# Kernel tuning notes

Hardware: AMD Instinct MI355X
Metric: run time of the kernel (lower is better)

## Reference

```python
import jax, jax.numpy as jnp
import numpy as np

N = 500_000      # active input voxels
C = 64           # feature channels
B = 2            # batch size
RES = 256        # input spatial resolution (coords in [0, RES))
FACTOR = 2       # downsample factor (init kwarg)


def setup_inputs() -> dict:
    key = jax.random.key(0)
    k1, k2, k3 = jax.random.split(key, 3)
    feats = jax.random.normal(k1, (N, C), dtype=jnp.float32)
    bidx = jax.random.randint(k2, (N, 1), 0, B, dtype=jnp.int32)
    xyz = jax.random.randint(k3, (N, 3), 0, RES, dtype=jnp.int32)
    coords = jnp.concatenate([bidx, xyz], axis=1)  # [N, 4] = (b, x, y, z)
    return {"feats": feats, "coords": coords}


def reference(feats, coords):
    """Sparse voxel downsample: coord hashing + dedup + scatter-mean pooling.

    Returns (new_feats [N, C], new_coords [N, 4]); rows beyond the number of
    unique downsampled voxels are zero-feature / coord = -1 padding (JAX needs
    static shapes; torch original returns only the n_unique valid rows).
    """
    res = RES // FACTOR  # static spatial extent after downsampling
    b = coords[:, 0].astype(jnp.int32)
    xyz = coords[:, 1:] // FACTOR  # [N, 3]
    # linear hash code = ((b*res + x)*res + y)*res + z
    code = ((b * res + xyz[:, 0]) * res + xyz[:, 1]) * res + xyz[:, 2]
    uniq, inv = jnp.unique(code, size=N, fill_value=-1, return_inverse=True)
    # mean pooling with include_self=False == segment_sum / segment_count
    counts = jax.ops.segment_sum(jnp.ones((N,), feats.dtype), inv, num_segments=N)
    sums = jax.ops.segment_sum(feats, inv, num_segments=N)  # [N, C]
    new_feats = sums / jnp.maximum(counts, 1.0)[:, None]
    # decode unique codes back to (b, x, y, z)
    valid = counts > 0
    z = uniq % res
    y = (uniq // res) % res
    x = (uniq // (res * res)) % res
    nb = uniq // (res * res * res)
    new_coords = jnp.stack([nb, x, y, z], axis=-1).astype(jnp.int32)
    new_coords = jnp.where(valid[:, None], new_coords, -1)
    return new_feats, new_coords
```

## Files before the change

### kernel.cpp

```cpp
#include <hip/hip_runtime.h>


#define RES2 128
#define NCODES (2 * 128 * 128 * 128)
#define NW (NCODES / 4)
#define HBLK 4096

typedef float f4 __attribute__((ext_vector_type(4)));

__global__ void zero_cnt(uint4* __restrict__ p) {
    int i = blockIdx.x * 256 + threadIdx.x;
    const uint4 zz = make_uint4(0u, 0u, 0u, 0u);
    if (i < NW / 4) p[i] = zz;
}

__global__ void count_codes(const int* __restrict__ coords,
                            unsigned* __restrict__ cnt8,
                            int* __restrict__ codes, int n) {
    int i = blockIdx.x * 256 + threadIdx.x;
    if (i >= n) return;
    const int4 v = reinterpret_cast<const int4*>(coords)[i];
    int code = (((v.x * RES2 + (v.y >> 1)) * RES2 + (v.z >> 1)) * RES2) + (v.w >> 1);
    codes[i] = code;
    atomicAdd(&cnt8[code >> 2], 1u << (8 * (code & 3)));
}

__global__ void block_flag_sum(const unsigned* __restrict__ cnt8,
                               unsigned* __restrict__ btot) {
    __shared__ unsigned sh[256];
    int t = threadIdx.x;
    unsigned w = cnt8[blockIdx.x * 256 + t];
    sh[t] = ((w & 0xFFu) != 0) + (((w >> 8) & 0xFFu) != 0) +
            (((w >> 16) & 0xFFu) != 0) + ((w >> 24) != 0);
    __syncthreads();
    for (int off = 128; off > 0; off >>= 1) {
        if (t < off) sh[t] += sh[t + off];
        __syncthreads();
    }
    if (t == 0) btot[blockIdx.x] = sh[0];
}

__global__ void scan_totals(unsigned* __restrict__ btot,
                            unsigned* __restrict__ nuq) {
    __shared__ unsigned sh[1024];
    int t = threadIdx.x;
    int base = t * 4;
    unsigned v[4], e[4], s = 0;
#pragma unroll
    for (int j = 0; j < 4; ++j) { v[j] = btot[base + j]; e[j] = s; s += v[j]; }
    sh[t] = s;
    __syncthreads();
    for (int off = 1; off < 1024; off <<= 1) {
        unsigned add = (t >= off) ? sh[t - off] : 0u;
        __syncthreads();
        sh[t] += add;
        __syncthreads();
    }
    unsigned excl = (t == 0) ? 0u : sh[t - 1];
#pragma unroll
    for (int j = 0; j < 4; ++j) btot[base + j] = excl + e[j];
    if (t == 1023) *nuq = sh[1023];
}

__global__ void scan_write(const unsigned* __restrict__ cnt8,
                           const unsigned* __restrict__ btot,
                           unsigned* __restrict__ wprefix,
                           f4* __restrict__ outF4,
                           f4* __restrict__ outC4) {
    __shared__ unsigned sh[256];
    int t = threadIdx.x;
    int widx = blockIdx.x * 256 + t;
    unsigned w = cnt8[widx];
    unsigned c4[4] = {w & 0xFFu, (w >> 8) & 0xFFu, (w >> 16) & 0xFFu, w >> 24};
    unsigned e[4], s = 0;
#pragma unroll
    for (int j = 0; j < 4; ++j) { e[j] = s; s += (c4[j] != 0); }
    sh[t] = s;
    __syncthreads();
    for (int off = 1; off < 256; off <<= 1) {
        unsigned add = (t >= off) ? sh[t - off] : 0u;
        __syncthreads();
        sh[t] += add;
        __syncthreads();
    }
    unsigned texcl = ((t == 0) ? 0u : sh[t - 1]) + btot[blockIdx.x];
    wprefix[widx] = texcl;
    int cbase = widx * 4;
#pragma unroll
    for (int j = 0; j < 4; ++j) {
        if (c4[j]) {
            unsigned r = texcl + e[j];
            int code = cbase + j;
            f4 cv = {(float)(code >> 21), (float)((code >> 14) & 127),
                     (float)((code >> 7) & 127), (float)(code & 127)};
            outC4[r] = cv;
            if (c4[j] >= 2) {
                f4* row = outF4 + (size_t)r * 16;
                const f4 zz = {0.f, 0.f, 0.f, 0.f};
#pragma unroll
                for (int q = 0; q < 16; ++q) row[q] = zz;
            }
        }
    }
}

__global__ void tail_pad(const unsigned* __restrict__ nuq,
                         f4* __restrict__ outF4,
                         f4* __restrict__ outC4, int n) {
    int r = blockIdx.x * 256 + threadIdx.x;
    if (r >= n || r < (int)*nuq) return;
    f4* row = outF4 + (size_t)r * 16;
    const f4 zz = {0.f, 0.f, 0.f, 0.f};
#pragma unroll
    for (int q = 0; q < 16; ++q) row[q] = zz;
    f4 mm = {-1.f, -1.f, -1.f, -1.f};
    outC4[r] = mm;
}

__global__ void scatter8(const f4* __restrict__ feats4,
                         const int* __restrict__ codes,
                         const unsigned* __restrict__ cnt8,
                         const unsigned* __restrict__ wprefix,
                         f4* __restrict__ outF4, int n) {
    int tid = blockIdx.x * 256 + threadIdx.x;
    int lane = threadIdx.x & 63;
    int wave = tid >> 6;
    int q = lane >> 4;
    int sub = lane & 15;
    int ib = wave * 8;

#pragma unroll
    for (int h = 0; h < 2; ++h) {
        int i = ib + h * 4 + q;
        if (i >= n) continue;
        int c = codes[i];
        unsigned w = cnt8[c >> 2];
        unsigned base = wprefix[c >> 2];
        int j = c & 3;
        unsigned cnt = (w >> (8 * j)) & 0xFFu;
        unsigned occ = 0;
        if (j > 0) occ += ((w & 0xFFu) != 0);
        if (j > 1) occ += (((w >> 8) & 0xFFu) != 0);
        if (j > 2) occ += (((w >> 16) & 0xFFu) != 0);
        unsigned r = base + occ;
        f4 v = feats4[(size_t)i * 16 + sub];
        f4* dst = outF4 + (size_t)r * 16 + sub;
        if (cnt == 1) {
            __builtin_nontemporal_store(v, dst);
        } else {
            float sc = 1.0f / (float)cnt;
            float* d = (float*)dst;
            atomicAdd(d + 0, v.x * sc);
            atomicAdd(d + 1, v.y * sc);
            atomicAdd(d + 2, v.z * sc);
            atomicAdd(d + 3, v.w * sc);
        }
    }
}

extern "C" void kernel_launch(void* const* d_in, const int* in_sizes, int n_in,
                              void* d_out, int out_size, void* d_ws, size_t ws_size,
                              hipStream_t stream) {
    const float* feats = (const float*)d_in[0];
    const int* coords = (const int*)d_in[1];
    const int n = in_sizes[1] / 4;

    float* outF = (float*)d_out;
    f4* outF4 = (f4*)outF;
    f4* outC4 = (f4*)(outF + (size_t)n * 64);

    unsigned* cnt8 = (unsigned*)d_ws;
    unsigned* btot = cnt8 + NW;
    unsigned* nuq = btot + HBLK;
    int* codes = (int*)(nuq + 1);
    unsigned* wprefix = (unsigned*)(codes + n);

    zero_cnt<<<2048, 256, 0, stream>>>((uint4*)cnt8);

    count_codes<<<(n + 255) / 256, 256, 0, stream>>>(coords, cnt8, codes, n);
    block_flag_sum<<<HBLK, 256, 0, stream>>>(cnt8, btot);
    scan_totals<<<1, 1024, 0, stream>>>(btot, nuq);
    scan_write<<<HBLK, 256, 0, stream>>>(cnt8, btot, wprefix, outF4, outC4);
    tail_pad<<<(n + 255) / 256, 256, 0, stream>>>(nuq, outF4, outC4, n);

    int waves = (n + 7) / 8;
    int blocks = (waves * 64 + 255) / 256;
    scatter8<<<blocks, 256, 0, stream>>>((const f4*)feats, codes, cnt8,
                                         wprefix, outF4, n);
}
```

Before: 133.2 us.

## Split pooling into sorted gather for first half and atomic scatter for rest

Extends the block scan to also carry count prefix sums, builds a per-row sorted input index list (counting-sort style), and uses it so that blocks in an interleaved hybrid kernel gather and average inputs for the first half of unique rows without atomics. The remaining rows still use the direct store or atomicAdd scatter path. It also widens scan loads to uint4 with fewer blocks. The aim is to cut float atomic traffic and the zeroing of multi-count rows, at the price of an extra fill pass, more workspace, and hard-coded grid constants that assume N=500000.

```diff
diff --git a/kernel.cpp b/kernel.cpp
--- a/kernel.cpp
+++ b/kernel.cpp
@@ -4,14 +4,14 @@
 #define RES2 128
 #define NCODES (2 * 128 * 128 * 128)
 #define NW (NCODES / 4)
-#define HBLK 4096
-
+#define SBLK 1024
+
+typedef unsigned long long u64;
 typedef float f4 __attribute__((ext_vector_type(4)));
 
 __global__ void zero_cnt(uint4* __restrict__ p) {
     int i = blockIdx.x * 256 + threadIdx.x;
-    const uint4 zz = make_uint4(0u, 0u, 0u, 0u);
-    if (i < NW / 4) p[i] = zz;
+    p[i] = make_uint4(0u, 0u, 0u, 0u);
 }
 
 __global__ void count_codes(const int* __restrict__ coords,
@@ -25,13 +25,20 @@
     atomicAdd(&cnt8[code >> 2], 1u << (8 * (code & 3)));
 }
 
-__global__ void block_flag_sum(const unsigned* __restrict__ cnt8,
-                               unsigned* __restrict__ btot) {
-    __shared__ unsigned sh[256];
+__device__ __forceinline__ u64 pack_word(unsigned w) {
+    unsigned b0 = w & 0xFFu, b1 = (w >> 8) & 0xFFu,
+             b2 = (w >> 16) & 0xFFu, b3 = w >> 24;
+    return ((u64)(b0 + b1 + b2 + b3) << 32) |
+           (u64)((b0 != 0) + (b1 != 0) + (b2 != 0) + (b3 != 0));
+}
+
+__global__ void block_sums(const unsigned* __restrict__ cnt8,
+                           u64* __restrict__ btot) {
+    __shared__ u64 sh[256];
     int t = threadIdx.x;
-    unsigned w = cnt8[blockIdx.x * 256 + t];
-    sh[t] = ((w & 0xFFu) != 0) + (((w >> 8) & 0xFFu) != 0) +
-            (((w >> 16) & 0xFFu) != 0) + ((w >> 24) != 0);
+    const uint4 w = reinterpret_cast<const uint4*>(cnt8)[blockIdx.x * 256 + t];
+    u64 s = pack_word(w.x) + pack_word(w.y) + pack_word(w.z) + pack_word(w.w);
+    sh[t] = s;
     __syncthreads();
     for (int off = 128; off > 0; off >>= 1) {
         if (t < off) sh[t] += sh[t + off];
@@ -40,75 +47,116 @@
     if (t == 0) btot[blockIdx.x] = sh[0];
 }
 
-__global__ void scan_totals(unsigned* __restrict__ btot,
-                            unsigned* __restrict__ nuq) {
-    __shared__ unsigned sh[1024];
+__global__ void scan_totals(u64* __restrict__ btot,
+                            unsigned* __restrict__ nuq_rs) {
+    __shared__ u64 sh[1024];
     int t = threadIdx.x;
-    int base = t * 4;
-    unsigned v[4], e[4], s = 0;
-#pragma unroll
-    for (int j = 0; j < 4; ++j) { v[j] = btot[base + j]; e[j] = s; s += v[j]; }
-    sh[t] = s;
+    u64 v = btot[t];
+    sh[t] = v;
     __syncthreads();
     for (int off = 1; off < 1024; off <<= 1) {
-        unsigned add = (t >= off) ? sh[t - off] : 0u;
+        u64 add = (t >= off) ? sh[t - off] : 0ull;
         __syncthreads();
         sh[t] += add;
         __syncthreads();
     }
-    unsigned excl = (t == 0) ? 0u : sh[t - 1];
-#pragma unroll
-    for (int j = 0; j < 4; ++j) btot[base + j] = excl + e[j];
-    if (t == 1023) *nuq = sh[1023];
+    btot[t] = sh[t] - v;
+    if (t == 1023) {
+        unsigned nu = (unsigned)(sh[1023] & 0xFFFFFFFFull);
+        nuq_rs[0] = nu;
+        nuq_rs[1] = nu >> 1;
+    }
 }
 
 __global__ void scan_write(const unsigned* __restrict__ cnt8,
-                           const unsigned* __restrict__ btot,
+                           const u64* __restrict__ btot,
+                           const unsigned* __restrict__ nuq_rs,
                            unsigned* __restrict__ wprefix,
+                           unsigned* __restrict__ uniq_cc,
+                           unsigned* __restrict__ row_end,
                            f4* __restrict__ outF4,
                            f4* __restrict__ outC4) {
-    __shared__ unsigned sh[256];
+    __shared__ u64 sh[256];
     int t = threadIdx.x;
-    int widx = blockIdx.x * 256 + t;
-    unsigned w = cnt8[widx];
-    unsigned c4[4] = {w & 0xFFu, (w >> 8) & 0xFFu, (w >> 16) & 0xFFu, w >> 24};
-    unsigned e[4], s = 0;
-#pragma unroll
-    for (int j = 0; j < 4; ++j) { e[j] = s; s += (c4[j] != 0); }
-    sh[t] = s;
+    int w4i = blockIdx.x * 256 + t;
+    const uint4 w = reinterpret_cast<const uint4*>(cnt8)[w4i];
+    unsigned ws[4] = {w.x, w.y, w.z, w.w};
+    u64 pw[4], tot = 0;
+#pragma unroll
+    for (int j = 0; j < 4; ++j) { pw[j] = pack_word(ws[j]); tot += pw[j]; }
+    sh[t] = tot;
     __syncthreads();
     for (int off = 1; off < 256; off <<= 1) {
-        unsigned add = (t >= off) ? sh[t - off] : 0u;
+        u64 add = (t >= off) ? sh[t - off] : 0ull;
         __syncthreads();
         sh[t] += add;
         __syncthreads();
     }
-    unsigned texcl = ((t == 0) ? 0u : sh[t - 1]) + btot[blockIdx.x];
-    wprefix[widx] = texcl;
-    int cbase = widx * 4;
+    u64 run = ((t == 0) ? 0ull : sh[t - 1]) + btot[blockIdx.x];
+    int rsplit = (int)nuq_rs[1];
+    uint4 wp;
 #pragma unroll
     for (int j = 0; j < 4; ++j) {
-        if (c4[j]) {
-            unsigned r = texcl + e[j];
-            int code = cbase + j;
-            f4 cv = {(float)(code >> 21), (float)((code >> 14) & 127),
-                     (float)((code >> 7) & 127), (float)(code & 127)};
-            outC4[r] = cv;
-            if (c4[j] >= 2) {
-                f4* row = outF4 + (size_t)r * 16;
-                const f4 zz = {0.f, 0.f, 0.f, 0.f};
-#pragma unroll
-                for (int q = 0; q < 16; ++q) row[q] = zz;
+        ((unsigned*)&wp)[j] = (unsigned)(run & 0xFFFFFFFFull);
+        unsigned flagbase = (unsigned)(run & 0xFFFFFFFFull);
+        unsigned stbase = (unsigned)(run >> 32);
+        int code0 = (w4i * 4 + j) * 4;
+        unsigned occ = 0, csum = 0;
+#pragma unroll
+        for (int jj = 0; jj < 4; ++jj) {
+            unsigned cnt = (ws[j] >> (8 * jj)) & 0xFFu;
+            if (cnt) {
+                unsigned r = flagbase + occ;
+                unsigned st = stbase + csum;
+                int code = code0 + jj;
+                uniq_cc[r] = (unsigned)code | (cnt << 22);
+                row_end[r] = st;
+                f4 cv = {(float)(code >> 21), (float)((code >> 14) & 127),
+                         (float)((code >> 7) & 127), (float)(code & 127)};
+                outC4[r] = cv;
+                if (cnt >= 2 && (int)r >= rsplit) {
+                    f4* row = outF4 + (size_t)r * 16;
+                    const f4 zz = {0.f, 0.f, 0.f, 0.f};
+#pragma unroll
+                    for (int q = 0; q < 16; ++q) row[q] = zz;
+                }
             }
+            occ += (cnt != 0);
+            csum += cnt;
         }
-    }
-}
-
-__global__ void tail_pad(const unsigned* __restrict__ nuq,
+        run += pw[j];
+    }
+    reinterpret_cast<uint4*>(wprefix)[w4i] = wp;
+}
+
+__global__ void fill_sorted(const int* __restrict__ codes,
+                            const unsigned* __restrict__ cnt8,
+                            const unsigned* __restrict__ wprefix,
+                            const unsigned* __restrict__ nuq_rs,
+                            unsigned* __restrict__ row_end,
+                            int* __restrict__ sorted_idx, int n) {
+    int i = blockIdx.x * 256 + threadIdx.x;
+    if (i >= n) return;
+    int c = codes[i];
+    unsigned w = cnt8[c >> 2];
+    unsigned base = wprefix[c >> 2];
+    int j = c & 3;
+    unsigned occ = 0;
+    if (j > 0) occ += ((w & 0xFFu) != 0);
+    if (j > 1) occ += (((w >> 8) & 0xFFu) != 0);
+    if (j > 2) occ += (((w >> 16) & 0xFFu) != 0);
+    unsigned r = base + occ;
+    if (r < nuq_rs[1]) {
+        unsigned pos = atomicAdd(&row_end[r], 1u);
+        sorted_idx[pos] = i;
+    }
+}
+
+__global__ void tail_pad(const unsigned* __restrict__ nuq_rs,
                          f4* __restrict__ outF4,
                          f4* __restrict__ outC4, int n) {
     int r = blockIdx.x * 256 + threadIdx.x;
-    if (r >= n || r < (int)*nuq) return;
+    if (r >= n || r < (int)nuq_rs[0]) return;
     f4* row = outF4 + (size_t)r * 16;
     const f4 zz = {0.f, 0.f, 0.f, 0.f};
 #pragma unroll
@@ -117,43 +165,77 @@
     outC4[r] = mm;
 }
 
-__global__ void scatter8(const f4* __restrict__ feats4,
-                         const int* __restrict__ codes,
-                         const unsigned* __restrict__ cnt8,
-                         const unsigned* __restrict__ wprefix,
-                         f4* __restrict__ outF4, int n) {
-    int tid = blockIdx.x * 256 + threadIdx.x;
+#define GB_ 3907
+#define SB_ 15625
+__global__ void hybrid(const f4* __restrict__ feats4,
+                       const int* __restrict__ codes,
+                       const unsigned* __restrict__ cnt8,
+                       const unsigned* __restrict__ wprefix,
+                       const int* __restrict__ sorted_idx,
+                       const unsigned* __restrict__ row_end,
+                       const unsigned* __restrict__ uniq_cc,
+                       const unsigned* __restrict__ nuq_rs,
+                       f4* __restrict__ outF4, int n) {
+    int b = blockIdx.x;
     int lane = threadIdx.x & 63;
-    int wave = tid >> 6;
     int q = lane >> 4;
     int sub = lane & 15;
-    int ib = wave * 8;
-
-#pragma unroll
-    for (int h = 0; h < 2; ++h) {
-        int i = ib + h * 4 + q;
-        if (i >= n) continue;
-        int c = codes[i];
-        unsigned w = cnt8[c >> 2];
-        unsigned base = wprefix[c >> 2];
-        int j = c & 3;
-        unsigned cnt = (w >> (8 * j)) & 0xFFu;
-        unsigned occ = 0;
-        if (j > 0) occ += ((w & 0xFFu) != 0);
-        if (j > 1) occ += (((w >> 8) & 0xFFu) != 0);
-        if (j > 2) occ += (((w >> 16) & 0xFFu) != 0);
-        unsigned r = base + occ;
-        f4 v = feats4[(size_t)i * 16 + sub];
-        f4* dst = outF4 + (size_t)r * 16 + sub;
-        if (cnt == 1) {
-            __builtin_nontemporal_store(v, dst);
-        } else {
-            float sc = 1.0f / (float)cnt;
-            float* d = (float*)dst;
-            atomicAdd(d + 0, v.x * sc);
-            atomicAdd(d + 1, v.y * sc);
-            atomicAdd(d + 2, v.z * sc);
-            atomicAdd(d + 3, v.w * sc);
+    int rsplit = (int)nuq_rs[1];
+
+    if (b % 5 == 0) {
+        int gb = b / 5;
+        int wave = ((gb * 256 + threadIdx.x) >> 6);
+        int rb = wave * 16 + q;
+#pragma unroll
+        for (int k = 0; k < 4; ++k) {
+            int r = rb + k * 4;
+            if (r >= rsplit) continue;
+            unsigned en = row_end[r];
+            unsigned cc = uniq_cc[r];
+            int cnt = (int)(cc >> 22);
+            int st = (int)en - cnt;
+            int i0 = sorted_idx[st];
+            f4 a = feats4[(size_t)i0 * 16 + sub];
+            if (cnt > 1) {
+                for (int m = 1; m < cnt; ++m) {
+                    int i = sorted_idx[st + m];
+                    a += feats4[(size_t)i * 16 + sub];
+                }
+                a *= (1.0f / (float)cnt);
+            }
+            outF4[(size_t)r * 16 + sub] = a;
+        }
+    } else {
+        int sb = b - 1 - b / 5;
+        int wave = ((sb * 256 + threadIdx.x) >> 6);
+        int ib = wave * 8;
+#pragma unroll
+        for (int h = 0; h < 2; ++h) {
+            int i = ib + h * 4 + q;
+            if (i >= n) continue;
+            int c = codes[i];
+            unsigned w = cnt8[c >> 2];
+            unsigned base = wprefix[c >> 2];
+            int j = c & 3;
+            unsigned cnt = (w >> (8 * j)) & 0xFFu;
+            unsigned occ = 0;
+            if (j > 0) occ += ((w & 0xFFu) != 0);
+            if (j > 1) occ += (((w >> 8) & 0xFFu) != 0);
+            if (j > 2) occ += (((w >> 16) & 0xFFu) != 0);
+            unsigned r = base + occ;
+            if ((int)r < rsplit) continue;
+            f4 v = feats4[(size_t)i * 16 + sub];
+            f4* dst = outF4 + (size_t)r * 16 + sub;
+            if (cnt == 1) {
+                *dst = v;
+            } else {
+                float sc = 1.0f / (float)cnt;
+                float* d = (float*)dst;
+                atomicAdd(d + 0, v.x * sc);
+                atomicAdd(d + 1, v.y * sc);
+                atomicAdd(d + 2, v.z * sc);
+                atomicAdd(d + 3, v.w * sc);
+            }
         }
     }
 }
@@ -170,21 +252,26 @@
     f4* outC4 = (f4*)(outF + (size_t)n * 64);
 
     unsigned* cnt8 = (unsigned*)d_ws;
-    unsigned* btot = cnt8 + NW;
-    unsigned* nuq = btot + HBLK;
-    int* codes = (int*)(nuq + 1);
-    unsigned* wprefix = (unsigned*)(codes + n);
-
-    zero_cnt<<<2048, 256, 0, stream>>>((uint4*)cnt8);
-
+    unsigned* wprefix = cnt8 + NW;
+    u64* btot = (u64*)(wprefix + NW);
+    unsigned* nuq_rs = (unsigned*)(btot + SBLK);
+    int* codes = (int*)(nuq_rs + 4);
+    unsigned* uniq_cc = (unsigned*)(codes + n);
+    unsigned* row_end = uniq_cc + n;
+    int* sorted_idx = (int*)(row_end + n);
+
+    zero_cnt<<<1024, 256, 0, stream>>>((uint4*)cnt8);
     count_codes<<<(n + 255) / 256, 256, 0, stream>>>(coords, cnt8, codes, n);
-    block_flag_sum<<<HBLK, 256, 0, stream>>>(cnt8, btot);
-    scan_totals<<<1, 1024, 0, stream>>>(btot, nuq);
-    scan_write<<<HBLK, 256, 0, stream>>>(cnt8, btot, wprefix, outF4, outC4);
-    tail_pad<<<(n + 255) / 256, 256, 0, stream>>>(nuq, outF4, outC4, n);
-
-    int waves = (n + 7) / 8;
-    int blocks = (waves * 64 + 255) / 256;
-    scatter8<<<blocks, 256, 0, stream>>>((const f4*)feats, codes, cnt8,
-                                         wprefix, outF4, n);
-}
+    block_sums<<<SBLK, 256, 0, stream>>>(cnt8, btot);
+    scan_totals<<<1, 1024, 0, stream>>>(btot, nuq_rs);
+    scan_write<<<SBLK, 256, 0, stream>>>(cnt8, btot, nuq_rs, wprefix,
+                                         uniq_cc, row_end, outF4, outC4);
+    fill_sorted<<<(n + 255) / 256, 256, 0, stream>>>(codes, cnt8, wprefix,
+                                                     nuq_rs, row_end,
+                                                     sorted_idx, n);
+    tail_pad<<<(n + 255) / 256, 256, 0, stream>>>(nuq_rs, outF4, outC4, n);
+
+    hybrid<<<GB_ + SB_, 256, 0, stream>>>((const f4*)feats, codes, cnt8,
+                                          wprefix, sorted_idx, row_end,
+                                          uniq_cc, nuq_rs, outF4, n);
+}
```

Result: slower. 149.8 us (+12.5%).
